# Optimization experiments

Hardware: AMD Instinct MI355X
Metric: run time of the kernel (lower is better)

The kernel has to match this reference:

```python
import jax, jax.numpy as jnp
import numpy as np
from jax import lax

EMB_SIZE = 50000   # word vocab
CHAR_SIZE = 2048   # distinct character images
E = 128            # emb_dimension
B = 1024           # batch
W = 6              # context words per center word
CPW = 5            # chars per word (LSTM seq len, hard-coded by expand(5,...))
DA = 128           # attention hidden dim
NEG = 5            # neg_num hard negatives
IMG = 38           # ((38-2)//2 - 2)//2 = 8 -> 32*8*8 = 2048 flat features
BN_EPS = 1e-5


def _u(key, shape, r):
    return jax.random.uniform(key, shape, jnp.float32, -r, r)


def setup_inputs():
    key = jax.random.key(0)
    ks = iter(jax.random.split(key, 40))
    r = 1.0 / E
    return dict(
        pos_u=jax.random.randint(next(ks), (B,), 0, EMB_SIZE),
        pos_v=jax.random.randint(next(ks), (B, W), 0, EMB_SIZE),
        noise_words=jax.random.randint(next(ks), (B, B // 2), 0, EMB_SIZE),
        wordid2charid=jax.random.randint(next(ks), (EMB_SIZE, CPW), 0, CHAR_SIZE),
        img_data=jax.random.normal(next(ks), (CHAR_SIZE, 1, IMG, IMG), jnp.float32),
        u_emb=_u(next(ks), (EMB_SIZE, E), r),
        v_emb=_u(next(ks), (EMB_SIZE, E), r),
        c1w=_u(next(ks), (32, 1, 3, 3), 1e-4), c1b=jnp.zeros((32,)),
        g1=jnp.ones((32,)), b1=jnp.zeros((32,)),
        c2w=_u(next(ks), (32, 32, 3, 3), 1e-2), c2b=jnp.zeros((32,)),
        g2=jnp.ones((32,)), b2=jnp.zeros((32,)),
        fcw=_u(next(ks), (E, 32 * 64), r), fcb=jnp.zeros((E,)),
        g3=jnp.ones((E,)), b3=jnp.zeros((E,)),
        wi_f=_u(next(ks), (4 * E, E), r), wh_f=_u(next(ks), (4 * E, E), r),
        bi_f=jnp.zeros((4 * E,)), bh_f=jnp.zeros((4 * E,)),
        wi_b=_u(next(ks), (4 * E, E), r), wh_b=_u(next(ks), (4 * E, E), r),
        bi_b=jnp.zeros((4 * E,)), bh_b=jnp.zeros((4 * E,)),
        a1w=_u(next(ks), (DA, 2 * E), r), a1b=jnp.zeros((DA,)),
        a2w=_u(next(ks), (1, DA), r), a2b=jnp.zeros((1,)),
        a3w=_u(next(ks), (E, 2 * E), r), a3b=jnp.zeros((E,)),
    )


def _bn2d(x, g, b):  # training-mode batchnorm, biased variance
    m = x.mean((0, 2, 3), keepdims=True)
    v = x.var((0, 2, 3), keepdims=True)
    return (x - m) / jnp.sqrt(v + BN_EPS) * g[None, :, None, None] + b[None, :, None, None]


def _bn1d(x, g, b):
    m = x.mean(0)
    v = x.var(0)
    return (x - m) / jnp.sqrt(v + BN_EPS) * g + b


def _maxpool2(x):  # NCHW 2x2 stride-2
    return lax.reduce_window(x, -jnp.inf, lax.max, (1, 1, 2, 2), (1, 1, 2, 2), 'VALID')


def _cnn(x, c1w, c1b, g1, b1, c2w, c2b, g2, b2, fcw, fcb, g3, b3):
    dn = ('NCHW', 'OIHW', 'NCHW')
    x = lax.conv_general_dilated(x, c1w, (1, 1), 'VALID', dimension_numbers=dn) + c1b[None, :, None, None]
    x = _maxpool2(_bn2d(x, g1, b1))
    x = lax.conv_general_dilated(x, c2w, (1, 1), 'VALID', dimension_numbers=dn) + c2b[None, :, None, None]
    x = _maxpool2(_bn2d(x, g2, b2))
    x = x.reshape(x.shape[0], -1)  # [N, 2048]
    x = x @ fcw.T + fcb
    return jax.nn.relu(_bn1d(x, g3, b3))


def _lstm_dir(x, wi, wh, bi, bh):  # x: [T, N, E] -> hs [T, N, H]
    H = wh.shape[1]
    N = x.shape[1]

    def step(carry, xt):
        h, c = carry
        g = xt @ wi.T + h @ wh.T + bi + bh
        i, f, gg, o = jnp.split(g, 4, axis=-1)
        c = jax.nn.sigmoid(f) * c + jax.nn.sigmoid(i) * jnp.tanh(gg)
        h = jax.nn.sigmoid(o) * jnp.tanh(c)
        return (h, c), h

    init = (jnp.zeros((N, H), x.dtype), jnp.zeros((N, H), x.dtype))
    _, hs = lax.scan(step, init, x)
    return hs


def _bilstm_att(x, wi_f, wh_f, bi_f, bh_f, wi_b, wh_b, bi_b, bh_b, a1w, a1b, a2w, a2b, a3w, a3b):
    hf = _lstm_dir(x, wi_f, wh_f, bi_f, bh_f)
    hb = _lstm_dir(x[::-1], wi_b, wh_b, bi_b, bh_b)[::-1]
    out = jnp.concatenate([hf, hb], axis=-1)          # [T, N, 2H]
    a = jnp.tanh(out @ a1w.T + a1b) @ a2w.T + a2b     # [T, N, 1]
    a = jax.nn.softmax(a, axis=0)                     # softmax over time (dim=0)
    y = (a * out).sum(0)                              # [N, 2H]
    return y @ a3w.T + a3b                            # [N, E]


def _forward(pos_u, pos_v, noise_words, wordid2charid, img_data, u_emb, v_emb,
             c1w, c1b, g1, b1, c2w, c2b, g2, b2, fcw, fcb, g3, b3,
             wi_f, wh_f, bi_f, bh_f, wi_b, wh_b, bi_b, bh_b,
             a1w, a1b, a2w, a2b, a3w, a3b):
    Bb, Ww = pos_v.shape
    img_emb = _cnn(img_data, c1w, c1b, g1, b1, c2w, c2b, g2, b2, fcw, fcb, g3, b3)  # [CHAR_SIZE, E]

    emb_u = u_emb[pos_u]                       # [B, E]
    emb_v = v_emb[pos_v].mean(1)               # [B, E]

    # forward_noise_strong_avg: cosine-sim topk hard-negative mining
    noise_vec = v_emb[noise_words]             # [B, M, E]
    num = jnp.einsum('be,bme->bm', emb_v, noise_vec)
    den = jnp.maximum(jnp.linalg.norm(emb_v, axis=-1)[:, None] * jnp.linalg.norm(noise_vec, axis=-1), 1e-8)
    cos = num / den
    _, idx = lax.top_k(cos, NEG)                                       # [B, NEG]
    neg_ids = jnp.take_along_axis(noise_words, idx, axis=1)            # [B, NEG]
    emb_neg_v = jnp.take_along_axis(noise_vec, idx[:, :, None], axis=1)  # [B, NEG, E]

    def char_ctx(word_ids):  # [n] -> [n, E]
        chars = wordid2charid[word_ids]         # [n, CPW]
        x = img_emb[chars]                      # [n, CPW, E]
        return _bilstm_att(jnp.swapaxes(x, 0, 1), wi_f, wh_f, bi_f, bh_f,
                           wi_b, wh_b, bi_b, bh_b, a1w, a1b, a2w, a2b, a3w, a3b)

    emb_char_v = char_ctx(pos_v.reshape(-1)).reshape(Bb, Ww, E).mean(1)   # [B, E]
    emb_neg_char_v = char_ctx(neg_ids.reshape(-1)).reshape(Bb, NEG, E)    # [B, NEG, E]

    def nls(s):
        return -jax.nn.log_sigmoid(jnp.clip(s, -10.0, 10.0))

    c_score = nls((emb_u * emb_char_v).sum(1))
    neg_c = -(jax.nn.log_sigmoid(-jnp.clip(jnp.einsum('bne,be->bn', emb_neg_char_v, emb_u), -10.0, 10.0))).sum(1)
    score = nls((emb_u * emb_v).sum(1))
    neg_s = -(jax.nn.log_sigmoid(-jnp.clip(jnp.einsum('bne,be->bn', emb_neg_v, emb_u), -10.0, 10.0))).sum(1)
    return jnp.mean(c_score + neg_c + score + neg_s)


def reference(pos_u, pos_v, noise_words, wordid2charid, img_data, u_emb, v_emb,
              c1w, c1b, g1, b1, c2w, c2b, g2, b2, fcw, fcb, g3, b3,
              wi_f, wh_f, bi_f, bh_f, wi_b, wh_b, bi_b, bh_b,
              a1w, a1b, a2w, a2b, a3w, a3b):
    return _forward(pos_u, pos_v, noise_words, wordid2charid, img_data, u_emb, v_emb,
                    c1w, c1b, g1, b1, c2w, c2b, g2, b2, fcw, fcb, g3, b3,
                    wi_f, wh_f, bi_f, bh_f, wi_b, wh_b, bi_b, bh_b,
                    a1w, a1b, a2w, a2b, a3w, a3b)
```

## Files before the change

kernel.cpp:

```cpp
#include <hip/hip_runtime.h>
#include <math.h>

#define NIMG   2048
#define EMB    128
#define NB     1024
#define WCTX   6
#define CPW    5
#define NEG    5
#define MNOISE 512
#define NWRD   11264
#define NPOSW  6144
#define TT     5

typedef __bf16 bf16x8 __attribute__((ext_vector_type(8)));
typedef float  f32x4  __attribute__((ext_vector_type(4)));
typedef float  f32x16 __attribute__((ext_vector_type(16)));

__device__ __forceinline__ float sigf(float x){ return __fdividef(1.0f, 1.0f+__expf(-x)); }
__device__ __forceinline__ float ftanh(float x){
  float xc = fminf(15.f, fmaxf(-15.f, x));
  float t = __expf(2.f*xc);
  return __fdividef(t - 1.f, t + 1.f);
}
__device__ __forceinline__ float splus(float z){
  return (z > 0.0f) ? z + log1pf(expf(-z)) : log1pf(expf(z));
}
__device__ __forceinline__ float clip10(float x){ return fminf(10.0f, fmaxf(-10.0f, x)); }
__device__ __forceinline__ float wsum64(float v){
  #pragma unroll
  for (int m = 1; m < 64; m <<= 1) v += __shfl_xor(v, m);
  return v;
}
__device__ __forceinline__ unsigned short f2b(float x){
  union { float f; unsigned u; } v; v.f = x;
  unsigned r = v.u + 0x7fff + ((v.u >> 16) & 1);
  return (unsigned short)(r >> 16);
}
__device__ __forceinline__ float b2f(unsigned short h){
  union { unsigned u; float f; } v; v.u = ((unsigned)h) << 16; return v.f;
}
__device__ __forceinline__ bf16x8 as_bf(uint4 u){
  union { uint4 q; bf16x8 v; } c; c.q = u; return c.v;
}

__global__ void k_prep(
  const float* __restrict__ wi_f, const float* __restrict__ wh_f,
  const float* __restrict__ wi_b, const float* __restrict__ wh_b,
  const float* __restrict__ a1w, const float* __restrict__ a3w,
  const float* __restrict__ c2w,
  const float* __restrict__ bi_f, const float* __restrict__ bh_f,
  const float* __restrict__ bi_b, const float* __restrict__ bh_b,
  const float* __restrict__ a2b, const float* __restrict__ v_emb,
  const int* __restrict__ pos_v, const int* __restrict__ w2c,
  unsigned short* __restrict__ wpf, unsigned short* __restrict__ wpb,
  unsigned short* __restrict__ a1p, unsigned short* __restrict__ a3p,
  unsigned short* __restrict__ c2p,
  float* __restrict__ bsf, float* __restrict__ bsb, float* __restrict__ sbuf,
  float* __restrict__ vbuf, float* __restrict__ vnorm,
  int* __restrict__ chars, float* __restrict__ st, float* __restrict__ scacc,
  float* __restrict__ fcout, float* __restrict__ norms2, int nvocab)
{
  int id = blockIdx.x*256 + threadIdx.x;
  if (id < 262144){
    int dir = id >> 17;
    int lid = id & 131071;
    const float* wi = dir ? wi_b : wi_f;
    const float* wh = dir ? wh_b : wh_f;
    unsigned short* out = dir ? wpb : wpf;
    int j = lid&7, l = (lid>>3)&63, p = (lid>>9)&31, s = lid>>14;
    int wn = p>>3, nf = p&7;
    int gate = nf&3, jb = wn*2 + (nf>>2);
    int n = gate*128 + jb*16 + (l&15);
    int k = s*32 + ((l>>4)<<3) + j;
    float v = (k < 128) ? wi[n*128+k] : wh[n*128 + (k-128)];
    out[lid] = f2b(v);
  } else if (id < 327680){
    int lid = id - 262144;
    int seg = lid >> 15;
    int pid = lid & 32767;
    const float* W = seg ? a3w : a1w;
    unsigned short* out = seg ? a3p : a1p;
    int j = pid&7, l = (pid>>3)&63, rest = pid>>9;
    int p = rest & 7, s = rest >> 3;
    int n = p*16 + (l&15);
    int k = s*32 + ((l>>4)<<3) + j;
    out[pid] = f2b(W[n*256 + k]);
  } else if (id < 336896){
    int pid = id - 327680;
    int j = pid & 7, l = (pid >> 3) & 63, p = (pid >> 9) & 1, t9 = pid >> 10;
    int oc = p*16 + (l & 15), ic = ((l >> 4) << 3) + j;
    c2p[pid] = f2b(c2w[oc*288 + ic*9 + t9]);
  } else if (id < 337408){
    int i = id - 336896;
    bsf[i] = bi_f[i] + bh_f[i];
    bsb[i] = bi_b[i] + bh_b[i];
  } else if (id < 393728){
    int i = id - 337408;
    sbuf[i] = a2b[0];
  } else if (id < 459264){
    int b = (id - 393728) >> 6;
    int l = id & 63;
    float s0 = 0.f, s1 = 0.f;
    for (int w = 0; w < WCTX; w++){
      int vid = pos_v[b*WCTX + w];
      s0 += v_emb[(size_t)vid*128 + l];
      s1 += v_emb[(size_t)vid*128 + 64 + l];
    }
    s0 *= (1.f/6.f); s1 *= (1.f/6.f);
    vbuf[b*128 + l] = s0; vbuf[b*128 + 64 + l] = s1;
    float nn = wsum64(s0*s0 + s1*s1);
    if (l == 0) vnorm[b] = sqrtf(nn);
  } else if (id < 489984){
    int i = id - 459264;
    int wi_ = i / CPW, t = i - wi_*CPW;
    chars[i] = w2c[pos_v[wi_]*CPW + t];
  } else if (id < 491008){
    st[id - 489984] = 0.f;
  } else if (id < 494464){
    scacc[id - 491008] = 0.f;
  } else if (id < 756608){
    fcout[id - 494464] = 0.f;
  } else if (id < 1556608){
    int lid = id - 756608;
    int row = lid >> 4, s = id & 15;
    if (row < nvocab){
      const float4* vp = (const float4*)(v_emb + (size_t)row*128 + s*8);
      float4 x0 = vp[0], x1 = vp[1];
      float q = x0.x*x0.x + x0.y*x0.y + x0.z*x0.z + x0.w*x0.w
              + x1.x*x1.x + x1.y*x1.y + x1.z*x1.z + x1.w*x1.w;
      q += __shfl_xor(q, 1); q += __shfl_xor(q, 2);
      q += __shfl_xor(q, 4); q += __shfl_xor(q, 8);
      if (s == 0) norms2[row] = q;
    }
  }
}

__global__ __launch_bounds__(256) void k_stats1(
    const float* __restrict__ img, float* __restrict__ SC)
{
  __shared__ float im[1444];
  __shared__ float SCw[4][54];
  int tid = threadIdx.x;
  float S[9], C[45];
  #pragma unroll
  for (int a = 0; a < 9; a++) S[a] = 0.f;
  #pragma unroll
  for (int a = 0; a < 45; a++) C[a] = 0.f;
  for (int ii = 0; ii < 4; ii++){
    int n = blockIdx.x*4 + ii;
    const float* ip = img + (size_t)n*1444;
    __syncthreads();
    for (int i = tid; i < 1444; i += 256) im[i] = ip[i];
    __syncthreads();
    for (int p = tid; p < 1296; p += 256){
      int oh = p/36, ow = p - oh*36;
      float P[9];
      #pragma unroll
      for (int i = 0; i < 3; i++)
        #pragma unroll
        for (int j = 0; j < 3; j++)
          P[i*3+j] = im[(oh+i)*38 + ow + j];
      int idx = 0;
      #pragma unroll
      for (int a = 0; a < 9; a++){
        S[a] += P[a];
        #pragma unroll
        for (int b = a; b < 9; b++){ C[idx] += P[a]*P[b]; idx++; }
      }
    }
  }
  #pragma unroll
  for (int a = 0; a < 9; a++) S[a] = wsum64(S[a]);
  #pragma unroll
  for (int a = 0; a < 45; a++) C[a] = wsum64(C[a]);
  if ((tid & 63) == 0){
    int w = tid >> 6;
    #pragma unroll
    for (int a = 0; a < 9; a++) SCw[w][a] = S[a];
    #pragma unroll
    for (int a = 0; a < 45; a++) SCw[w][9+a] = C[a];
  }
  __syncthreads();
  if (tid < 54){
    float v = SCw[0][tid] + SCw[1][tid] + SCw[2][tid] + SCw[3][tid];
    atomicAdd(&SC[tid*64 + (blockIdx.x & 63)], v);
  }
}

__global__ void k_fold1(const float* __restrict__ SC, const float* __restrict__ c1w,
                        const float* __restrict__ c1b, const float* __restrict__ g1,
                        const float* __restrict__ b1,
                        unsigned short* __restrict__ c1p, float* __restrict__ bias1c,
                        float* __restrict__ stp)
{
  __shared__ float S[9], C[45];
  __shared__ float scs[32];
  int tid = threadIdx.x;
  #pragma unroll
  for (int k = 0; k < 64; k++) stp[k*64 + tid] = 0.f;
  if (tid < 54){
    float acc = 0.f;
    for (int s = 0; s < 64; s++) acc += SC[tid*64 + s];
    if (tid < 9) S[tid] = acc; else C[tid-9] = acc;
  }
  __syncthreads();
  if (tid < 32){
    const float invN = 1.0f/2654208.0f;
    float w[9];
    #pragma unroll
    for (int a = 0; a < 9; a++) w[a] = c1w[tid*9+a];
    float b = c1b[tid];
    float sum = 0.f;
    #pragma unroll
    for (int a = 0; a < 9; a++) sum += w[a]*S[a];
    float sq = 0.f; int idx = 0;
    #pragma unroll
    for (int a = 0; a < 9; a++)
      #pragma unroll
      for (int bb_ = a; bb_ < 9; bb_++){
        float f = (bb_ == a) ? w[a]*w[a] : 2.f*w[a]*w[bb_];
        sq += f*C[idx]; idx++;
      }
    float Epre = sum*invN;
    float var = sq*invN - Epre*Epre;
    float m = Epre + b;
    float sc = g1[tid]*rsqrtf(var + 1e-5f);
    scs[tid] = sc;
    bias1c[tid] = sc*b + (b1[tid] - m*sc);
  }
  __syncthreads();
  {
    int l = tid;
    int ch = l & 31;
    float sc = scs[ch];
    #pragma unroll
    for (int j = 0; j < 8; j++){
      int k = ((l >> 5) << 3) + j;
      int kh = k >> 2, kw = k & 3;
      float v = (kh < 3 && kw < 3) ? c1w[ch*9 + kh*3 + kw]*sc : 0.f;
      c1p[l*8+j] = f2b(v);
    }
  }
}

__global__ __launch_bounds__(512) void k_conv12(
    const float* __restrict__ img, const unsigned short* __restrict__ c1p,
    const float* __restrict__ bias1c, const unsigned short* __restrict__ c2pack,
    const float* __restrict__ c2b,
    unsigned short* __restrict__ flat2, float* __restrict__ stp)
{
  __shared__ __align__(16) unsigned short Ai[1520];
  __shared__ __align__(16) unsigned short Bi[1520];
  __shared__ __align__(16) unsigned short Pt[324*32];
  __shared__ float lsum[32], lsq[32];
  int n = blockIdx.x, tid = threadIdx.x;
  if (tid < 190){
    int r = tid/5, c = tid - r*5;
    if (c < 2) Ai[r*40 + 38 + c] = 0;
    else       Bi[r*40 + 37 + (c-2)] = 0;
  }
  if (tid >= 192 && tid < 224){ lsum[tid-192] = 0.f; }
  if (tid >= 224 && tid < 256){ lsq[tid-224] = 0.f; }
  const float4* ip4 = (const float4*)(img + (size_t)n*1444);
  for (int i = tid; i < 361; i += 512){
    float4 v = ip4[i];
    int flat = i*4;
    const float* pv = (const float*)&v;
    #pragma unroll
    for (int e = 0; e < 4; e++){
      int f = flat + e;
      int r = f / 38, c = f - r*38;
      unsigned short h = f2b(pv[e]);
      Ai[r*40 + c] = h;
      if (c) Bi[r*40 + c - 1] = h;
    }
  }
  __syncthreads();
  int l = tid & 63, w = tid >> 6;
  {
    int hi = l >> 5;
    int ch = l & 31;
    int r31 = l & 31;
    int member = r31 & 3;
    const unsigned short* P = (member & 1) ? Bi : Ai;
    int rowoff = (member >> 1) * 40;
    bf16x8 bw = as_bf(*(const uint4*)(c1p + (size_t)l*8));
    float bias = bias1c[ch];
    int inoff = (ch & 7)*2;
    int chgrp = ch >> 3;
    #pragma unroll 2
    for (int g = w; g < 41; g += 8){
      int ql = g*8 + (r31 >> 2);
      if (ql > 323) ql = 323;
      int ph = ql/18, pw = ql - ph*18;
      int off = (2*ph)*40 + rowoff + 2*pw;
      uint4 a = (uint4){0u,0u,0u,0u};
      if (hi == 0){
        const unsigned* p0 = (const unsigned*)(P + off);
        const unsigned* p1 = (const unsigned*)(P + off + 40);
        a.x = p0[0]; a.y = p0[1]; a.z = p1[0]; a.w = p1[1];
      } else {
        const unsigned* p2 = (const unsigned*)(P + off + 80);
        a.x = p2[0]; a.y = p2[1];
      }
      f32x16 acc = __builtin_amdgcn_mfma_f32_32x32x16_bf16(
          as_bf(a), bw,
          (f32x16){0.f,0.f,0.f,0.f,0.f,0.f,0.f,0.f,0.f,0.f,0.f,0.f,0.f,0.f,0.f,0.f},
          0, 0, 0);
      #pragma unroll
      for (int rg = 0; rg < 4; rg++){
        int qo = g*8 + rg*2 + hi;
        if (qo < 324){
          float v0 = acc[rg*4+0]+bias, v1 = acc[rg*4+1]+bias;
          float v2 = acc[rg*4+2]+bias, v3 = acc[rg*4+3]+bias;
          float mx = fmaxf(fmaxf(v0,v1), fmaxf(v2,v3));
          *(unsigned short*)((char*)Pt + qo*64 + (((chgrp ^ (qo & 3)) << 4) + inoff)) = f2b(mx);
        }
      }
    }
  }
  __syncthreads();
  int wid = w;
  int wM = wid >> 1, wN = wid & 1;
  bf16x8 bfr[9];
  #pragma unroll
  for (int t9 = 0; t9 < 9; t9++)
    bfr[t9] = as_bf(*(const uint4*)(c2pack + ((size_t)(t9*2 + wN)*64 + l)*8));
  f32x4 acc[4];
  #pragma unroll
  for (int mf = 0; mf < 4; mf++) acc[mf] = (f32x4){0.f,0.f,0.f,0.f};
  #pragma unroll
  for (int t9 = 0; t9 < 9; t9++){
    int kh = t9/3, kw = t9 - (t9/3)*3;
    #pragma unroll
    for (int mf = 0; mf < 4; mf++){
      int pos = wM*64 + mf*16 + (l & 15);
      int oh = pos >> 4, ow = pos & 15;
      int q = (oh + kh)*18 + (ow + kw);
      int slot = ((l >> 4) ^ q) & 3;
      bf16x8 a = as_bf(*(const uint4*)((const char*)Pt + q*64 + slot*16));
      acc[mf] = __builtin_amdgcn_mfma_f32_16x16x32_bf16(a, bfr[t9], acc[mf], 0, 0, 0);
    }
  }
  int oc = wN*16 + (l & 15);
  int qq = l >> 4;
  float bb = c2b[oc];
  float vm[4][4];
  float s = 0.f, sq = 0.f;
  #pragma unroll
  for (int mf = 0; mf < 4; mf++)
    #pragma unroll
    for (int reg = 0; reg < 4; reg++){
      float v = acc[mf][reg] + bb;
      vm[mf][reg] = v;
      s += v; sq += v*v;
    }
  s += __shfl_xor(s,16); sq += __shfl_xor(sq,16);
  s += __shfl_xor(s,32); sq += __shfl_xor(sq,32);
  if (qq == 0){ atomicAdd(&lsum[oc], s); atomicAdd(&lsq[oc], sq); }
  unsigned short* fp = flat2 + (size_t)n*2048 + oc*64;
  #pragma unroll
  for (int mp = 0; mp < 2; mp++){
    int ph = wM*2 + mp;
    float p0 = fmaxf(fmaxf(vm[2*mp][0], vm[2*mp][1]), fmaxf(vm[2*mp+1][0], vm[2*mp+1][1]));
    float p1 = fmaxf(fmaxf(vm[2*mp][2], vm[2*mp][3]), fmaxf(vm[2*mp+1][2], vm[2*mp+1][3]));
    unsigned pk = ((unsigned)f2b(p1) << 16) | (unsigned)f2b(p0);
    *(unsigned*)(fp + ph*8 + qq*2) = pk;
  }
  __syncthreads();
  if (tid < 32){
    int slot = (blockIdx.x & 63)*64;
    atomicAdd(&stp[slot + tid], lsum[tid]);
    atomicAdd(&stp[slot + 32 + tid], lsq[tid]);
  }
}

__global__ void k_fold2(const float* __restrict__ stp, float* __restrict__ st)
{
  int v = threadIdx.x;
  float acc = 0.f;
  #pragma unroll 8
  for (int s = 0; s < 64; s++) acc += stp[s*64 + v];
  st[128 + v] = acc;
}

__global__ void k_fcscale(const float* __restrict__ fcw, const float* __restrict__ st,
                          const float* __restrict__ g2, unsigned short* __restrict__ fcp)
{
  int id = blockIdx.x*256 + threadIdx.x;
  if (id >= 262144) return;
  int j = id&7, l = (id>>3)&63, rest = id>>9;
  int p = rest & 7, s = rest >> 3;
  int n = p*16 + (l&15);
  int k = s*32 + ((l>>4)<<3) + j;
  int c = k >> 6;
  float m = st[128+c]*(1.f/524288.f);
  float var = st[160+c]*(1.f/524288.f) - m*m;
  float sc = g2[c]*rsqrtf(var + 1e-5f);
  fcp[id] = f2b(fcw[(size_t)n*2048 + k] * sc);
}

__global__ __launch_bounds__(512) void k_gemm_mfma(
    const unsigned short* __restrict__ A0, const unsigned short* __restrict__ A1,
    const unsigned short* __restrict__ wpack, const float* __restrict__ bias,
    float* __restrict__ out, const float* __restrict__ a2w, float* __restrict__ sbuf,
    int M, int K, int fuse)
{
  __shared__ unsigned short At[64*256];
  __shared__ float wt[64][5];
  int tid = threadIdx.x;
  int l = tid & 63, wid = tid >> 6;
  int row0 = blockIdx.x * 64;
  int wm = wid >> 2, wn = wid & 3;
  int kspan = K / gridDim.y;
  int kbeg = blockIdx.y * kspan;
  f32x4 acc[2][2];
  #pragma unroll
  for (int a = 0; a < 2; a++)
    #pragma unroll
    for (int b = 0; b < 2; b++) acc[a][b] = (f32x4){0.f,0.f,0.f,0.f};

  if (fuse == 3){
    if (tid < 64){
      int gr = row0 + tid;
      float sv[TT];
      float mx = -1e30f;
      #pragma unroll
      for (int t = 0; t < TT; t++){ sv[t] = sbuf[t*NWRD + gr]; mx = fmaxf(mx, sv[t]); }
      float sum = 0.f;
      #pragma unroll
      for (int t = 0; t < TT; t++){ sv[t] = __expf(sv[t] - mx); sum += sv[t]; }
      float inv = __fdividef(1.f, sum);
      #pragma unroll
      for (int t = 0; t < TT; t++) wt[tid][t] = sv[t]*inv;
    }
    __syncthreads();
  }

  for (int kc = kbeg; kc < kbeg + kspan; kc += 256){
    #pragma unroll
    for (int it = 0; it < 4; it++){
      int ci = tid + 512*it;
      int r = ci >> 5, c = ci & 31;
      int gr = row0 + r; int k = kc + c*8;
      uint4 v;
      if (fuse == 3){
        int col = (k < 128) ? k : (k - 128);
        const unsigned short* sp = (k < 128) ? A0 : A1;
        float a8[8];
        #pragma unroll
        for (int e = 0; e < 8; e++) a8[e] = 0.f;
        #pragma unroll
        for (int t = 0; t < TT; t++){
          uint4 hv = *(const uint4*)(sp + ((size_t)t*NWRD + gr)*128 + col);
          const unsigned short* ph = (const unsigned short*)&hv;
          float wgt = wt[r][t];
          #pragma unroll
          for (int e = 0; e < 8; e++) a8[e] += wgt * b2f(ph[e]);
        }
        unsigned short o[8];
        #pragma unroll
        for (int e = 0; e < 8; e++) o[e] = f2b(a8[e]);
        v = *(uint4*)o;
      } else {
        const unsigned short* src;
        if (A1) src = (k < 128) ? (A0 + (size_t)gr*128 + k) : (A1 + (size_t)gr*128 + (k-128));
        else    src = A0 + (size_t)gr*K + k;
        v = *(const uint4*)src;
      }
      *(uint4*)((char*)At + r*512 + ((c*16) ^ ((r & 7) << 4))) = v;
    }
    __syncthreads();
    #pragma unroll
    for (int s8 = 0; s8 < 8; s8++){
      int s = (kc >> 5) + s8;
      bf16x8 af[2];
      #pragma unroll
      for (int mf = 0; mf < 2; mf++){
        int r = wm*32 + mf*16 + (l & 15);
        int cb = (s8*4 + (l >> 4)) ^ (r & 7);
        af[mf] = as_bf(*(const uint4*)((const char*)At + r*512 + cb*16));
      }
      #pragma unroll
      for (int nf = 0; nf < 2; nf++){
        bf16x8 bf_ = as_bf(*(const uint4*)(wpack + ((size_t)(s*8 + wn*2 + nf)*64 + l)*8));
        acc[0][nf] = __builtin_amdgcn_mfma_f32_16x16x32_bf16(af[0], bf_, acc[0][nf], 0,0,0);
        acc[1][nf] = __builtin_amdgcn_mfma_f32_16x16x32_bf16(af[1], bf_, acc[1][nf], 0,0,0);
      }
    }
    __syncthreads();
  }
  if (fuse == 0 || fuse == 3){
    #pragma unroll
    for (int mf = 0; mf < 2; mf++)
      #pragma unroll
      for (int nf = 0; nf < 2; nf++)
        #pragma unroll
        for (int reg = 0; reg < 4; reg++){
          int row = row0 + wm*32 + mf*16 + ((l >> 4) << 2) + reg;
          int col = wn*32 + nf*16 + (l & 15);
          out[(size_t)row*128 + col] = acc[mf][nf][reg] + bias[col];
        }
  } else if (fuse == 2){
    #pragma unroll
    for (int mf = 0; mf < 2; mf++)
      #pragma unroll
      for (int nf = 0; nf < 2; nf++)
        #pragma unroll
        for (int reg = 0; reg < 4; reg++){
          int row = row0 + wm*32 + mf*16 + ((l >> 4) << 2) + reg;
          int col = wn*32 + nf*16 + (l & 15);
          atomicAdd(&out[(size_t)row*128 + col], acc[mf][nf][reg]);
        }
  } else {
    float part[2][4];
    #pragma unroll
    for (int mf = 0; mf < 2; mf++)
      #pragma unroll
      for (int reg = 0; reg < 4; reg++){
        float p = 0.f;
        #pragma unroll
        for (int nf = 0; nf < 2; nf++){
          int col = wn*32 + nf*16 + (l & 15);
          p += ftanh(acc[mf][nf][reg] + bias[col]) * a2w[col];
        }
        part[mf][reg] = p;
      }
    #pragma unroll
    for (int msk = 1; msk < 16; msk <<= 1)
      #pragma unroll
      for (int mf = 0; mf < 2; mf++)
        #pragma unroll
        for (int reg = 0; reg < 4; reg++)
          part[mf][reg] += __shfl_xor(part[mf][reg], msk);
    if ((l & 15) == 0){
      #pragma unroll
      for (int mf = 0; mf < 2; mf++)
        #pragma unroll
        for (int reg = 0; reg < 4; reg++)
          atomicAdd(&sbuf[row0 + wm*32 + mf*16 + ((l >> 4) << 2) + reg], part[mf][reg]);
    }
  }
}

__global__ __launch_bounds__(256) void k_bn1d_fused(const float* __restrict__ fc,
    const float* __restrict__ g3, const float* __restrict__ b3,
    unsigned short* __restrict__ img_emb)
{
  int j = blockIdx.x, tid = threadIdx.x;
  float vr[8];
  float s = 0.f, q = 0.f;
  #pragma unroll
  for (int u = 0; u < 8; u++){
    float v = fc[(u*256 + tid)*128 + j];
    vr[u] = v; s += v; q += v*v;
  }
  s = wsum64(s); q = wsum64(q);
  __shared__ float rs[4], rq[4];
  if ((tid & 63) == 0){ rs[tid>>6] = s; rq[tid>>6] = q; }
  __syncthreads();
  float S = rs[0]+rs[1]+rs[2]+rs[3];
  float Q = rq[0]+rq[1]+rq[2]+rq[3];
  float m = S*(1.f/2048.f);
  float var = Q*(1.f/2048.f) - m*m;
  float sc = g3[j]*rsqrtf(var + 1e-5f);
  float sh = b3[j] - m*sc;
  #pragma unroll
  for (int u = 0; u < 8; u++)
    img_emb[(u*256 + tid)*128 + j] = f2b(fmaxf(0.f, vr[u]*sc + sh));
}

__global__ __launch_bounds__(256) void k_xproj(
    const unsigned short* __restrict__ xemb,
    const unsigned short* __restrict__ wpf, const unsigned short* __restrict__ wpb,
    const float* __restrict__ bsf, const float* __restrict__ bsb,
    unsigned short* __restrict__ xgf, unsigned short* __restrict__ xgb)
{
  __shared__ unsigned short At[64*128];
  int dir = blockIdx.z;
  const unsigned short* wpack = dir ? wpb : wpf;
  const float* bsum = dir ? bsb : bsf;
  unsigned short* xg = dir ? xgb : xgf;
  int tid = threadIdx.x;
  int l = tid & 63, wid = tid >> 6;
  int row0 = blockIdx.x * 64;
  int wm = wid >> 1;
  int wn = blockIdx.y*2 + (wid & 1);
  #pragma unroll
  for (int it = 0; it < 4; it++){
    int ci = tid + 256*it;
    int r = ci >> 4, c = ci & 15;
    uint4 v = *(const uint4*)(xemb + (size_t)(row0 + r)*128 + c*8);
    *(uint4*)((char*)At + r*256 + ((c*16) ^ ((r & 7) << 4))) = v;
  }
  __syncthreads();
  f32x4 acc[2][8];
  #pragma unroll
  for (int a = 0; a < 2; a++)
    #pragma unroll
    for (int b = 0; b < 8; b++) acc[a][b] = (f32x4){0.f,0.f,0.f,0.f};
  #pragma unroll
  for (int s4 = 0; s4 < 4; s4++){
    bf16x8 af[2];
    #pragma unroll
    for (int mf = 0; mf < 2; mf++){
      int r = wm*32 + mf*16 + (l & 15);
      int cb = (s4*4 + (l >> 4)) ^ (r & 7);
      af[mf] = as_bf(*(const uint4*)((const char*)At + r*256 + cb*16));
    }
    #pragma unroll
    for (int nf = 0; nf < 8; nf++){
      bf16x8 bf_ = as_bf(*(const uint4*)(wpack + ((size_t)(s4*32 + wn*8 + nf)*64 + l)*8));
      acc[0][nf] = __builtin_amdgcn_mfma_f32_16x16x32_bf16(af[0], bf_, acc[0][nf], 0,0,0);
      acc[1][nf] = __builtin_amdgcn_mfma_f32_16x16x32_bf16(af[1], bf_, acc[1][nf], 0,0,0);
    }
  }
  #pragma unroll
  for (int mf = 0; mf < 2; mf++)
    #pragma unroll
    for (int reg = 0; reg < 4; reg++){
      int gr = row0 + wm*32 + mf*16 + ((l >> 4) << 2) + reg;
      unsigned short* xrow = xg + (size_t)gr*512;
      #pragma unroll
      for (int js = 0; js < 2; js++){
        int jl = wn*32 + js*16 + (l & 15);
        unsigned short o[4];
        o[0] = f2b(acc[mf][js*4+0][reg] + bsum[jl]);
        o[1] = f2b(acc[mf][js*4+1][reg] + bsum[128+jl]);
        o[2] = f2b(acc[mf][js*4+2][reg] + bsum[256+jl]);
        o[3] = f2b(acc[mf][js*4+3][reg] + bsum[384+jl]);
        *(uint2*)(xrow + jl*4) = *(uint2*)o;
      }
    }
}

__global__ __launch_bounds__(512, 4) void k_lstm5(
    const int* __restrict__ chars,
    const unsigned short* __restrict__ wpf, const unsigned short* __restrict__ wpb,
    const unsigned short* __restrict__ xgf, const unsigned short* __restrict__ xgb,
    unsigned short* __restrict__ hsf, unsigned short* __restrict__ hsb)
{
  __shared__ __align__(16) unsigned short At[2][2048];
  __shared__ int cid_s[80];
  int b = blockIdx.x;
  int br = b & 7;
  int dir = br >> 2;
  int rblk = (b >> 3)*4 + (br & 3);
  const unsigned short* wpack = dir ? wpb : wpf;
  const unsigned short* xg = dir ? xgb : xgf;
  unsigned short* hs = dir ? hsb : hsf;
  int tid = threadIdx.x;
  int l = tid & 63, c = tid >> 6;
  int jl = c*16 + (l & 15);
  int row0 = rblk * 16;

  if (tid < 80) cid_s[tid] = chars[row0*CPW + tid];

  bf16x8 wreg[4][4];
  #pragma unroll
  for (int s4 = 0; s4 < 4; s4++)
    #pragma unroll
    for (int g = 0; g < 4; g++)
      wreg[s4][g] = as_bf(*(const uint4*)(wpack + ((size_t)((s4+4)*32 + c*4 + g)*64 + l)*8));

  int frow = tid >> 5, fq = tid & 31;
  int fof = (((fq >> 1) ^ (frow & 7)) << 4) | ((fq & 1) << 3);

  __syncthreads();

  int rbase = (l >> 4) << 2;
  int t0 = dir ? (TT-1) : 0;
  uint2 xv[4], xvn[4];
  #pragma unroll
  for (int reg = 0; reg < 4; reg++)
    xv[reg] = *(const uint2*)(xg + (size_t)cid_s[(rbase+reg)*CPW + t0]*512 + jl*4);

  float creg[4];
  #pragma unroll
  for (int reg = 0; reg < 4; reg++) creg[reg] = 0.f;
  int tprev = t0;

  #pragma unroll
  for (int tF = 0; tF < TT; tF++){
    int t = dir ? (TT-1-tF) : tF;
    f32x4 acc[4];
    if (tF > 0){
      __syncthreads();
      const unsigned short* buf = At[(tF-1) & 1];
      uint2 hv = *(const uint2*)((const char*)buf + tid*8);
      {
        union { uint2 v; unsigned long long q; } cv; cv.v = hv;
        __builtin_nontemporal_store(cv.q,
          (unsigned long long*)((char*)(hs + (size_t)tprev*NWRD*128 + (size_t)(row0 + frow)*128) + fof));
      }
      if (tF + 1 < TT){
        int tn = dir ? (TT-2-tF) : (tF+1);
        #pragma unroll
        for (int reg = 0; reg < 4; reg++)
          xvn[reg] = *(const uint2*)(xg + (size_t)cid_s[(rbase+reg)*CPW + tn]*512 + jl*4);
      }
      #pragma unroll
      for (int g = 0; g < 4; g++) acc[g] = (f32x4){0.f,0.f,0.f,0.f};
      #pragma unroll
      for (int s4 = 0; s4 < 4; s4++){
        int r = l & 15;
        int cb = (s4*4 + (l >> 4)) ^ (r & 7);
        bf16x8 af = as_bf(*(const uint4*)((const char*)buf + r*256 + cb*16));
        #pragma unroll
        for (int g = 0; g < 4; g++)
          acc[g] = __builtin_amdgcn_mfma_f32_16x16x32_bf16(af, wreg[s4][g], acc[g], 0,0,0);
      }
    } else {
      int tn = dir ? (TT-2) : 1;
      #pragma unroll
      for (int reg = 0; reg < 4; reg++)
        xvn[reg] = *(const uint2*)(xg + (size_t)cid_s[(rbase+reg)*CPW + tn]*512 + jl*4);
      #pragma unroll
      for (int g = 0; g < 4; g++) acc[g] = (f32x4){0.f,0.f,0.f,0.f};
    }
    unsigned short* wb = At[tF & 1];
    #pragma unroll
    for (int reg = 0; reg < 4; reg++){
      int rloc = ((l >> 4) << 2) + reg;
      const unsigned short* xs = (const unsigned short*)&xv[reg];
      float ig = acc[0][reg] + b2f(xs[0]);
      float fg = acc[1][reg] + b2f(xs[1]);
      float gg = acc[2][reg] + b2f(xs[2]);
      float og = acc[3][reg] + b2f(xs[3]);
      float co = creg[reg];
      float ei = __expf(-__builtin_amdgcn_fmed3f(ig, -30.f, 30.f));
      float eg = __expf(2.f*__builtin_amdgcn_fmed3f(gg, -15.f, 15.f));
      float sf = __fdividef(1.f, 1.f + __expf(-__builtin_amdgcn_fmed3f(fg, -30.f, 30.f)));
      float itg = __fdividef(eg - 1.f, (1.f + ei)*(eg + 1.f));
      float cn = sf*co + itg;
      float eo = __expf(-__builtin_amdgcn_fmed3f(og, -30.f, 30.f));
      float ec = __expf(2.f*__builtin_amdgcn_fmed3f(cn, -15.f, 15.f));
      float h  = __fdividef(ec - 1.f, (1.f + eo)*(ec + 1.f));
      creg[reg] = cn;
      int byteoff = rloc*256 + ((((jl >> 3) << 4) ^ ((rloc & 7) << 4)) + (jl & 7)*2);
      *(unsigned short*)((char*)wb + byteoff) = f2b(h);
    }
    tprev = t;
    #pragma unroll
    for (int reg = 0; reg < 4; reg++) xv[reg] = xvn[reg];
  }
  __syncthreads();
  const unsigned short* buf = At[(TT-1) & 1];
  uint2 hv = *(const uint2*)((const char*)buf + tid*8);
  {
    union { uint2 v; unsigned long long q; } cv; cv.v = hv;
    __builtin_nontemporal_store(cv.q,
      (unsigned long long*)((char*)(hs + (size_t)tprev*NWRD*128 + (size_t)(row0 + frow)*128) + fof));
  }
}

__global__ __launch_bounds__(256) void k_cos2(const int* __restrict__ noise,
    const float* __restrict__ v_emb, const float* __restrict__ vbuf,
    const float* __restrict__ vnorm, const float* __restrict__ norms2,
    float* __restrict__ cosb)
{
  int b = blockIdx.x;
  int tid = threadIdx.x;
  int s = tid & 15;
  int rsub = (tid >> 4) & 3;
  int wid = tid >> 6;
  const float4* ep = (const float4*)(vbuf + b*128 + s*8);
  float4 e0 = ep[0], e1 = ep[1];
  float nb = vnorm[b];
  int mbase = blockIdx.y*128 + wid*4 + rsub;
  #pragma unroll 4
  for (int iter = 0; iter < 8; iter++){
    int m = mbase + iter*16;
    int id = noise[b*MNOISE + m];
    const float4* vp = (const float4*)(v_emb + (size_t)id*128 + s*8);
    float4 x0 = vp[0], x1 = vp[1];
    float d = e0.x*x0.x + e0.y*x0.y + e0.z*x0.z + e0.w*x0.w
            + e1.x*x1.x + e1.y*x1.y + e1.z*x1.z + e1.w*x1.w;
    d += __shfl_xor(d, 1); d += __shfl_xor(d, 2);
    d += __shfl_xor(d, 4); d += __shfl_xor(d, 8);
    if (s == 0){
      float q = norms2[id];
      cosb[b*MNOISE + m] = d / fmaxf(nb*sqrtf(q), 1e-8f);
    }
  }
}

__global__ __launch_bounds__(64) void k_topk(const float* __restrict__ cosb,
    const int* __restrict__ noise, const int* __restrict__ w2c,
    int* __restrict__ neg_ids, int* __restrict__ chars)
{
  __shared__ int nid_s[NEG];
  int b = blockIdx.x, l = threadIdx.x;
  float v[8];
  int base = b*MNOISE;
  #pragma unroll
  for (int q = 0; q < 8; q++) v[q] = cosb[base + l + 64*q];
  for (int r = 0; r < NEG; r++){
    float bv = -1e30f; int bidx = 1<<30;
    #pragma unroll
    for (int q = 0; q < 8; q++){
      int idx = l + 64*q;
      if (v[q] > bv || (v[q] == bv && idx < bidx)){ bv = v[q]; bidx = idx; }
    }
    #pragma unroll
    for (int m = 1; m < 64; m <<= 1){
      float ov = __shfl_xor(bv, m);
      int   oi = __shfl_xor(bidx, m);
      if (ov > bv || (ov == bv && oi < bidx)){ bv = ov; bidx = oi; }
    }
    if (l == 0){
      int nid = noise[base + bidx];
      neg_ids[b*NEG + r] = nid;
      nid_s[r] = nid;
    }
    int qsel = bidx >> 6;
    #pragma unroll
    for (int q = 0; q < 8; q++)
      if (q == qsel && (bidx & 63) == l) v[q] = -1e30f;
  }
  __syncthreads();
  if (l < NEG*CPW){
    int k = l / CPW, t = l - k*CPW;
    chars[(NPOSW + b*NEG + k)*CPW + t] = w2c[nid_s[k]*CPW + t];
  }
}

__global__ __launch_bounds__(64) void k_loss(const int* __restrict__ pos_u,
    const float* __restrict__ u_emb, const float* __restrict__ vbuf,
    const float* __restrict__ echar, const int* __restrict__ neg_ids,
    const float* __restrict__ v_emb, float* __restrict__ part)
{
  int b = blockIdx.x, l = threadIdx.x;
  int pu = pos_u[b];
  float eu0 = u_emb[pu*128 + l], eu1 = u_emb[pu*128 + 64 + l];
  float c0 = 0.f, c1 = 0.f;
  for (int w = 0; w < WCTX; w++){
    int r = b*WCTX + w;
    c0 += echar[r*128 + l]; c1 += echar[r*128 + 64 + l];
  }
  c0 *= (1.f/6.f); c1 *= (1.f/6.f);
  float d1 = wsum64(eu0*c0 + eu1*c1);
  float d2 = wsum64(eu0*vbuf[b*128 + l] + eu1*vbuf[b*128 + 64 + l]);
  float tot = splus(-clip10(d1)) + splus(-clip10(d2));
  for (int k = 0; k < NEG; k++){
    int r = NPOSW + b*NEG + k;
    float dc = wsum64(eu0*echar[r*128 + l] + eu1*echar[r*128 + 64 + l]);
    int nid = neg_ids[b*NEG + k];
    float dn = wsum64(eu0*v_emb[nid*128 + l] + eu1*v_emb[nid*128 + 64 + l]);
    tot += splus(clip10(dc)) + splus(clip10(dn));
  }
  if (l == 0) part[b] = tot;
}

__global__ __launch_bounds__(256) void k_final(const float* __restrict__ part, float* __restrict__ out)
{
  int tid = threadIdx.x;
  float s = part[tid] + part[tid+256] + part[tid+512] + part[tid+768];
  s = wsum64(s);
  __shared__ float r[4];
  if ((tid & 63) == 0) r[tid>>6] = s;
  __syncthreads();
  if (tid == 0) out[0] = (r[0]+r[1]+r[2]+r[3]) * (1.0f/1024.0f);
}

extern "C" void kernel_launch(void* const* d_in, const int* in_sizes, int n_in,
                              void* d_out, int out_size, void* d_ws, size_t ws_size,
                              hipStream_t stream)
{
  (void)n_in; (void)out_size; (void)ws_size;
  const int*   pos_u  = (const int*)  d_in[0];
  const int*   pos_v  = (const int*)  d_in[1];
  const int*   noise  = (const int*)  d_in[2];
  const int*   w2c    = (const int*)  d_in[3];
  const float* img    = (const float*)d_in[4];
  const float* u_emb  = (const float*)d_in[5];
  const float* v_emb  = (const float*)d_in[6];
  const float* c1w    = (const float*)d_in[7];
  const float* c1b    = (const float*)d_in[8];
  const float* g1     = (const float*)d_in[9];
  const float* b1     = (const float*)d_in[10];
  const float* c2w    = (const float*)d_in[11];
  const float* c2b    = (const float*)d_in[12];
  const float* g2     = (const float*)d_in[13];
  const float* b2     = (const float*)d_in[14];
  const float* fcw    = (const float*)d_in[15];
  const float* fcb    = (const float*)d_in[16];
  const float* g3     = (const float*)d_in[17];
  const float* b3     = (const float*)d_in[18];
  const float* wi_f   = (const float*)d_in[19];
  const float* wh_f   = (const float*)d_in[20];
  const float* bi_f   = (const float*)d_in[21];
  const float* bh_f   = (const float*)d_in[22];
  const float* wi_b   = (const float*)d_in[23];
  const float* wh_b   = (const float*)d_in[24];
  const float* bi_b   = (const float*)d_in[25];
  const float* bh_b   = (const float*)d_in[26];
  const float* a1w    = (const float*)d_in[27];
  const float* a1b    = (const float*)d_in[28];
  const float* a2w    = (const float*)d_in[29];
  const float* a2b    = (const float*)d_in[30];
  const float* a3w    = (const float*)d_in[31];
  const float* a3b    = (const float*)d_in[32];
  (void)fcb; (void)b2;
  int nvocab = in_sizes[6] / 128;

  char* ws = (char*)d_ws;
  typedef unsigned short u16;
  constexpr size_t OFF_ST   = 0;
  constexpr size_t OFF_WPF  = 4096;
  constexpr size_t OFF_WPB  = OFF_WPF + 262144;
  constexpr size_t OFF_A1P  = OFF_WPB + 262144;
  constexpr size_t OFF_A3P  = OFF_A1P + 65536;
  constexpr size_t OFF_FCP  = OFF_A3P + 65536;
  constexpr size_t OFF_C2P  = OFF_FCP + 524288;
  constexpr size_t OFF_C1P  = OFF_C2P + 18432;
  constexpr size_t OFF_BSF  = OFF_C1P + 2048;
  constexpr size_t OFF_BSB  = OFF_BSF + 2048;
  constexpr size_t OFF_SC   = OFF_BSB + 2048;
  constexpr size_t OFF_HSF  = OFF_SC + 14336;
  constexpr size_t OFF_HSB  = OFF_HSF + 14417920;
  constexpr size_t OFF_FL2  = OFF_HSB + 14417920;
  constexpr size_t OFF_ECH  = OFF_FL2 + 5767168;
  constexpr size_t OFF_FC   = OFF_ECH + 5767168;
  constexpr size_t OFF_IE   = OFF_FC  + 1048576;
  constexpr size_t OFF_VB   = OFF_IE  + 524288;
  constexpr size_t OFF_VN   = OFF_VB  + 524288;
  constexpr size_t OFF_COS  = OFF_VN  + 4096;
  constexpr size_t OFF_NI   = OFF_COS + 2097152;
  constexpr size_t OFF_CH   = OFF_NI  + 20480;
  constexpr size_t OFF_SB   = OFF_CH  + 225280;
  constexpr size_t OFF_PART = OFF_SB  + 225280;
  constexpr size_t OFF_NRM  = OFF_PART + 4096;
  constexpr size_t OFF_XGF  = OFF_NRM + 204800;
  constexpr size_t OFF_XGB  = OFF_XGF + 2097152;

  float* st      = (float*)(ws + OFF_ST);
  u16*   wpf     = (u16*)  (ws + OFF_WPF);
  u16*   wpb     = (u16*)  (ws + OFF_WPB);
  u16*   a1p     = (u16*)  (ws + OFF_A1P);
  u16*   a3p     = (u16*)  (ws + OFF_A3P);
  u16*   fcp     = (u16*)  (ws + OFF_FCP);
  u16*   c2p     = (u16*)  (ws + OFF_C2P);
  u16*   c1p     = (u16*)  (ws + OFF_C1P);
  float* bsf     = (float*)(ws + OFF_BSF);
  float* bsb     = (float*)(ws + OFF_BSB);
  float* scacc   = (float*)(ws + OFF_SC);
  u16*   flat2   = (u16*)  (ws + OFF_FL2);
  float* fcout   = (float*)(ws + OFF_FC);
  u16*   imgemb  = (u16*)  (ws + OFF_IE);
  float* vbuf    = (float*)(ws + OFF_VB);
  float* vnorm   = (float*)(ws + OFF_VN);
  float* cosb    = (float*)(ws + OFF_COS);
  int*   negi    = (int*)  (ws + OFF_NI);
  int*   charsb  = (int*)  (ws + OFF_CH);
  u16*   hsf     = (u16*)  (ws + OFF_HSF);
  u16*   hsb     = (u16*)  (ws + OFF_HSB);
  float* sb      = (float*)(ws + OFF_SB);
  float* echar   = (float*)(ws + OFF_ECH);
  float* part    = (float*)(ws + OFF_PART);
  float* norms2  = (float*)(ws + OFF_NRM);
  u16*   xgf     = (u16*)  (ws + OFF_XGF);
  u16*   xgb     = (u16*)  (ws + OFF_XGB);
  float* stp     = (float*)(ws + OFF_COS);

  k_prep<<<6081, 256, 0, stream>>>(wi_f, wh_f, wi_b, wh_b, a1w, a3w, c2w,
                                   bi_f, bh_f, bi_b, bh_b, a2b, v_emb, pos_v, w2c,
                                   wpf, wpb, a1p, a3p, c2p, bsf, bsb, sb,
                                   vbuf, vnorm, charsb, st, scacc, fcout, norms2, nvocab);

  k_stats1<<<512, 256, 0, stream>>>(img, scacc);
  k_fold1<<<1, 64, 0, stream>>>(scacc, c1w, c1b, g1, b1, c1p, st+520, stp);
  k_conv12<<<NIMG, 512, 0, stream>>>(img, c1p, st+520, c2p, c2b, flat2, stp);
  k_fold2<<<1, 64, 0, stream>>>(stp, st);
  k_fcscale<<<1024, 256, 0, stream>>>(fcw, st, g2, fcp);
  k_gemm_mfma<<<dim3(32, 4), 512, 0, stream>>>(flat2, nullptr, fcp, nullptr, fcout,
                                               nullptr, nullptr, 2048, 2048, 2);
  k_bn1d_fused<<<128, 256, 0, stream>>>(fcout, g3, b3, imgemb);
  k_xproj<<<dim3(32, 2, 2), 256, 0, stream>>>(imgemb, wpf, wpb, bsf, bsb, xgf, xgb);

  k_cos2<<<dim3(NB, 4), 256, 0, stream>>>(noise, v_emb, vbuf, vnorm, norms2, cosb);
  k_topk<<<NB, 64, 0, stream>>>(cosb, noise, w2c, negi, charsb);

  k_lstm5<<<dim3(1408, 1, 1), 512, 0, stream>>>(charsb, wpf, wpb, xgf, xgb, hsf, hsb);

  k_gemm_mfma<<<TT*NWRD/64, 512, 0, stream>>>(hsf, hsb, a1p, a1b, nullptr, a2w, sb,
                                              TT*NWRD, 256, 1);
  k_gemm_mfma<<<NWRD/64, 512, 0, stream>>>(hsf, hsb, a3p, a3b, echar, nullptr, sb,
                                           NWRD, 256, 3);

  k_loss<<<NB, 64, 0, stream>>>(pos_u, u_emb, vbuf, echar, negi, v_emb, part);
  k_final<<<1, 256, 0, stream>>>(part, (float*)d_out);
}
```

Measured before the change: 207.9 us.

## Process two 16-row tiles per LSTM block to reuse register-held weights

Each LSTM block now handles 32 rows as two independent 16-row tiles that share the weight fragments kept in registers, and the grid is halved to match. This spreads the per-block weight load and the per-step barriers over twice the work and gives the scheduler two independent MFMA chains to interleave. In exchange it raises register and LDS use per block, which may lower occupancy, and it leaves fewer blocks to cover the GPU.

```diff
diff --git a/kernel.cpp b/kernel.cpp
--- a/kernel.cpp
+++ b/kernel.cpp
@@ -640,8 +640,8 @@
     const unsigned short* __restrict__ xgf, const unsigned short* __restrict__ xgb,
     unsigned short* __restrict__ hsf, unsigned short* __restrict__ hsb)
 {
-  __shared__ __align__(16) unsigned short At[2][2048];
-  __shared__ int cid_s[80];
+  __shared__ __align__(16) unsigned short At[2][2][2048];
+  __shared__ int cid_s[160];
   int b = blockIdx.x;
   int br = b & 7;
   int dir = br >> 2;
@@ -652,9 +652,9 @@
   int tid = threadIdx.x;
   int l = tid & 63, c = tid >> 6;
   int jl = c*16 + (l & 15);
-  int row0 = rblk * 16;
-
-  if (tid < 80) cid_s[tid] = chars[row0*CPW + tid];
+  int row0 = rblk * 32;
+
+  if (tid < 160) cid_s[tid] = chars[row0*CPW + tid];
 
   bf16x8 wreg[4][4];
   #pragma unroll
@@ -670,87 +670,107 @@
 
   int rbase = (l >> 4) << 2;
   int t0 = dir ? (TT-1) : 0;
-  uint2 xv[4], xvn[4];
-  #pragma unroll
-  for (int reg = 0; reg < 4; reg++)
-    xv[reg] = *(const uint2*)(xg + (size_t)cid_s[(rbase+reg)*CPW + t0]*512 + jl*4);
-
-  float creg[4];
-  #pragma unroll
-  for (int reg = 0; reg < 4; reg++) creg[reg] = 0.f;
+  uint2 xv[2][4], xvn[2][4];
+  #pragma unroll
+  for (int T = 0; T < 2; T++)
+    #pragma unroll
+    for (int reg = 0; reg < 4; reg++)
+      xv[T][reg] = *(const uint2*)(xg + (size_t)cid_s[(T*16 + rbase+reg)*CPW + t0]*512 + jl*4);
+
+  float creg[2][4];
+  #pragma unroll
+  for (int T = 0; T < 2; T++)
+    #pragma unroll
+    for (int reg = 0; reg < 4; reg++) creg[T][reg] = 0.f;
   int tprev = t0;
 
   #pragma unroll
   for (int tF = 0; tF < TT; tF++){
     int t = dir ? (TT-1-tF) : tF;
-    f32x4 acc[4];
+    f32x4 acc[2][4];
     if (tF > 0){
       __syncthreads();
-      const unsigned short* buf = At[(tF-1) & 1];
-      uint2 hv = *(const uint2*)((const char*)buf + tid*8);
-      {
+      #pragma unroll
+      for (int T = 0; T < 2; T++){
+        const unsigned short* buf = At[T][(tF-1) & 1];
+        uint2 hv = *(const uint2*)((const char*)buf + tid*8);
         union { uint2 v; unsigned long long q; } cv; cv.v = hv;
         __builtin_nontemporal_store(cv.q,
-          (unsigned long long*)((char*)(hs + (size_t)tprev*NWRD*128 + (size_t)(row0 + frow)*128) + fof));
+          (unsigned long long*)((char*)(hs + (size_t)tprev*NWRD*128 + (size_t)(row0 + T*16 + frow)*128) + fof));
       }
       if (tF + 1 < TT){
         int tn = dir ? (TT-2-tF) : (tF+1);
         #pragma unroll
-        for (int reg = 0; reg < 4; reg++)
-          xvn[reg] = *(const uint2*)(xg + (size_t)cid_s[(rbase+reg)*CPW + tn]*512 + jl*4);
-      }
-      #pragma unroll
-      for (int g = 0; g < 4; g++) acc[g] = (f32x4){0.f,0.f,0.f,0.f};
-      #pragma unroll
-      for (int s4 = 0; s4 < 4; s4++){
-        int r = l & 15;
-        int cb = (s4*4 + (l >> 4)) ^ (r & 7);
-        bf16x8 af = as_bf(*(const uint4*)((const char*)buf + r*256 + cb*16));
-        #pragma unroll
-        for (int g = 0; g < 4; g++)
-          acc[g] = __builtin_amdgcn_mfma_f32_16x16x32_bf16(af, wreg[s4][g], acc[g], 0,0,0);
+        for (int T = 0; T < 2; T++)
+          #pragma unroll
+          for (int reg = 0; reg < 4; reg++)
+            xvn[T][reg] = *(const uint2*)(xg + (size_t)cid_s[(T*16 + rbase+reg)*CPW + tn]*512 + jl*4);
+      }
+      #pragma unroll
+      for (int T = 0; T < 2; T++){
+        #pragma unroll
+        for (int g = 0; g < 4; g++) acc[T][g] = (f32x4){0.f,0.f,0.f,0.f};
+        #pragma unroll
+        for (int s4 = 0; s4 < 4; s4++){
+          int r = l & 15;
+          int cb = (s4*4 + (l >> 4)) ^ (r & 7);
+          bf16x8 af = as_bf(*(const uint4*)((const char*)At[T][(tF-1) & 1] + r*256 + cb*16));
+          #pragma unroll
+          for (int g = 0; g < 4; g++)
+            acc[T][g] = __builtin_amdgcn_mfma_f32_16x16x32_bf16(af, wreg[s4][g], acc[T][g], 0,0,0);
+        }
       }
     } else {
       int tn = dir ? (TT-2) : 1;
       #pragma unroll
-      for (int reg = 0; reg < 4; reg++)
-        xvn[reg] = *(const uint2*)(xg + (size_t)cid_s[(rbase+reg)*CPW + tn]*512 + jl*4);
-      #pragma unroll
-      for (int g = 0; g < 4; g++) acc[g] = (f32x4){0.f,0.f,0.f,0.f};
-    }
-    unsigned short* wb = At[tF & 1];
-    #pragma unroll
-    for (int reg = 0; reg < 4; reg++){
-      int rloc = ((l >> 4) << 2) + reg;
-      const unsigned short* xs = (const unsigned short*)&xv[reg];
-      float ig = acc[0][reg] + b2f(xs[0]);
-      float fg = acc[1][reg] + b2f(xs[1]);
-      float gg = acc[2][reg] + b2f(xs[2]);
-      float og = acc[3][reg] + b2f(xs[3]);
-      float co = creg[reg];
-      float ei = __expf(-__builtin_amdgcn_fmed3f(ig, -30.f, 30.f));
-      float eg = __expf(2.f*__builtin_amdgcn_fmed3f(gg, -15.f, 15.f));
-      float sf = __fdividef(1.f, 1.f + __expf(-__builtin_amdgcn_fmed3f(fg, -30.f, 30.f)));
-      float itg = __fdividef(eg - 1.f, (1.f + ei)*(eg + 1.f));
-      float cn = sf*co + itg;
-      float eo = __expf(-__builtin_amdgcn_fmed3f(og, -30.f, 30.f));
-      float ec = __expf(2.f*__builtin_amdgcn_fmed3f(cn, -15.f, 15.f));
-      float h  = __fdividef(ec - 1.f, (1.f + eo)*(ec + 1.f));
-      creg[reg] = cn;
-      int byteoff = rloc*256 + ((((jl >> 3) << 4) ^ ((rloc & 7) << 4)) + (jl & 7)*2);
-      *(unsigned short*)((char*)wb + byteoff) = f2b(h);
+      for (int T = 0; T < 2; T++)
+        #pragma unroll
+        for (int reg = 0; reg < 4; reg++)
+          xvn[T][reg] = *(const uint2*)(xg + (size_t)cid_s[(T*16 + rbase+reg)*CPW + tn]*512 + jl*4);
+      #pragma unroll
+      for (int T = 0; T < 2; T++)
+        #pragma unroll
+        for (int g = 0; g < 4; g++) acc[T][g] = (f32x4){0.f,0.f,0.f,0.f};
+    }
+    #pragma unroll
+    for (int T = 0; T < 2; T++){
+      unsigned short* wb = At[T][tF & 1];
+      #pragma unroll
+      for (int reg = 0; reg < 4; reg++){
+        int rloc = ((l >> 4) << 2) + reg;
+        const unsigned short* xs = (const unsigned short*)&xv[T][reg];
+        float ig = acc[T][0][reg] + b2f(xs[0]);
+        float fg = acc[T][1][reg] + b2f(xs[1]);
+        float gg = acc[T][2][reg] + b2f(xs[2]);
+        float og = acc[T][3][reg] + b2f(xs[3]);
+        float co = creg[T][reg];
+        float ei = __expf(-__builtin_amdgcn_fmed3f(ig, -30.f, 30.f));
+        float eg = __expf(2.f*__builtin_amdgcn_fmed3f(gg, -15.f, 15.f));
+        float sf = __fdividef(1.f, 1.f + __expf(-__builtin_amdgcn_fmed3f(fg, -30.f, 30.f)));
+        float itg = __fdividef(eg - 1.f, (1.f + ei)*(eg + 1.f));
+        float cn = sf*co + itg;
+        float eo = __expf(-__builtin_amdgcn_fmed3f(og, -30.f, 30.f));
+        float ec = __expf(2.f*__builtin_amdgcn_fmed3f(cn, -15.f, 15.f));
+        float h  = __fdividef(ec - 1.f, (1.f + eo)*(ec + 1.f));
+        creg[T][reg] = cn;
+        int byteoff = rloc*256 + ((((jl >> 3) << 4) ^ ((rloc & 7) << 4)) + (jl & 7)*2);
+        *(unsigned short*)((char*)wb + byteoff) = f2b(h);
+      }
     }
     tprev = t;
     #pragma unroll
-    for (int reg = 0; reg < 4; reg++) xv[reg] = xvn[reg];
-  }
-  __syncthreads();
-  const unsigned short* buf = At[(TT-1) & 1];
-  uint2 hv = *(const uint2*)((const char*)buf + tid*8);
-  {
+    for (int T = 0; T < 2; T++)
+      #pragma unroll
+      for (int reg = 0; reg < 4; reg++) xv[T][reg] = xvn[T][reg];
+  }
+  __syncthreads();
+  #pragma unroll
+  for (int T = 0; T < 2; T++){
+    const unsigned short* buf = At[T][(TT-1) & 1];
+    uint2 hv = *(const uint2*)((const char*)buf + tid*8);
     union { uint2 v; unsigned long long q; } cv; cv.v = hv;
     __builtin_nontemporal_store(cv.q,
-      (unsigned long long*)((char*)(hs + (size_t)tprev*NWRD*128 + (size_t)(row0 + frow)*128) + fof));
+      (unsigned long long*)((char*)(hs + (size_t)tprev*NWRD*128 + (size_t)(row0 + T*16 + frow)*128) + fof));
   }
 }
 
@@ -981,7 +1001,7 @@
   k_cos2<<<dim3(NB, 4), 256, 0, stream>>>(noise, v_emb, vbuf, vnorm, norms2, cosb);
   k_topk<<<NB, 64, 0, stream>>>(cosb, noise, w2c, negi, charsb);
 
-  k_lstm5<<<dim3(1408, 1, 1), 512, 0, stream>>>(charsb, wpf, wpb, xgf, xgb, hsf, hsb);
+  k_lstm5<<<dim3(704, 1, 1), 512, 0, stream>>>(charsb, wpf, wpb, xgf, xgb, hsf, hsb);
 
   k_gemm_mfma<<<TT*NWRD/64, 512, 0, stream>>>(hsf, hsb, a1p, a1b, nullptr, a2w, sb,
                                               TT*NWRD, 256, 1);
```

Result: slower. 257.4 us (+23.8%).
